# Kernel optimization log

Hardware: AMD Instinct MI355X
Metric: run time of the kernel (lower is better)

The kernel has to match this reference:

```python
import jax, jax.numpy as jnp
import numpy as np
from jax import lax

B, S, I, H, O, L = 64, 1024, 256, 1024, 256, 2


def setup_inputs() -> dict:
    key = jax.random.key(0)
    ks = iter(jax.random.split(key, 64))
    d = {}
    d["x"] = jax.random.normal(next(ks), (B, S, I), dtype=jnp.float32)
    d["h0"] = jnp.zeros((B, L, H), dtype=jnp.float32)
    for l in range(L):
        ind = I if l == 0 else H
        sx = 1.0 / np.sqrt(ind)
        sh = 1.0 / np.sqrt(H)
        d[f"Wxz_{l}"] = jax.random.uniform(next(ks), (ind, H), jnp.float32, -sx, sx)
        d[f"Wxr_{l}"] = jax.random.uniform(next(ks), (ind, H), jnp.float32, -sx, sx)
        d[f"Wxg_{l}"] = jax.random.uniform(next(ks), (ind, H), jnp.float32, -sx, sx)
        d[f"Whz_{l}"] = jax.random.uniform(next(ks), (H, H), jnp.float32, -sh, sh)
        d[f"bhz_{l}"] = jax.random.uniform(next(ks), (H,), jnp.float32, -sh, sh)
        d[f"Whr_{l}"] = jax.random.uniform(next(ks), (H, H), jnp.float32, -sh, sh)
        d[f"bhr_{l}"] = jax.random.uniform(next(ks), (H,), jnp.float32, -sh, sh)
        d[f"Whg_{l}"] = jax.random.uniform(next(ks), (H, H), jnp.float32, -sh, sh)
        d[f"bhg_{l}"] = jax.random.uniform(next(ks), (H,), jnp.float32, -sh, sh)
    sy = 1.0 / np.sqrt(H)
    d["WY"] = jax.random.uniform(next(ks), (H, O), jnp.float32, -sy, sy)
    d["bY"] = jax.random.uniform(next(ks), (O,), jnp.float32, -sy, sy)
    return d


def _gru_forward(x, h0, layer_params, WY, bY):
    # x: [B,S,I], h0: [B,L,H]
    def step(states, xt):
        inp = xt  # [B, in_dim]
        new_states = []
        for l, (wxz, wxr, wxg, whz, bhz, whr, bhr, whg, bhg) in enumerate(layer_params):
            h = states[l]
            z = jax.nn.sigmoid(inp @ wxz + h @ whz + bhz)
            r = jax.nn.sigmoid(inp @ wxr + h @ whr + bhr)
            g = jnp.tanh(inp @ wxg + (r * h) @ whg + bhg)
            h = z * h + (1.0 - z) * g
            new_states.append(h)
            inp = h  # dropout=0 -> identity
        y = inp @ WY + bY
        return tuple(new_states), y

    states0 = tuple(h0[:, l, :] for l in range(len(layer_params)))
    xs = jnp.swapaxes(x, 0, 1)  # [S,B,I]
    final_states, ys = lax.scan(step, states0, xs)
    layer_output = jnp.swapaxes(ys, 0, 1)  # [B,S,O]
    hidden_state = jnp.stack(final_states, axis=1)  # [B,L,H]
    return layer_output, hidden_state


def reference(x, h0,
              Wxz_0, Wxr_0, Wxg_0, Whz_0, bhz_0, Whr_0, bhr_0, Whg_0, bhg_0,
              Wxz_1, Wxr_1, Wxg_1, Whz_1, bhz_1, Whr_1, bhr_1, Whg_1, bhg_1,
              WY, bY):
    layer_params = [
        (Wxz_0, Wxr_0, Wxg_0, Whz_0, bhz_0, Whr_0, bhr_0, Whg_0, bhg_0),
        (Wxz_1, Wxr_1, Wxg_1, Whz_1, bhz_1, Whr_1, bhr_1, Whg_1, bhg_1),
    ]
    return _gru_forward(x, h0, layer_params, WY, bY)
```

## Files before the change

### kernel.cpp

```cpp
#include <hip/hip_runtime.h>
#include <hip/hip_bf16.h>
#include <stdint.h>


#define NWG 200
#define TPB 256

typedef unsigned long long u64;
typedef __attribute__((ext_vector_type(8))) short bfrag;
typedef __attribute__((ext_vector_type(4))) float f32x4;

constexpr int Bc = 64, Sc = 1024, Ic = 256, Hc = 1024, Oc = 256;

struct Args {
  const float *x, *h0in;
  const float *W1[7], *W2[7], *bias[7];
  unsigned short *h0[2], *h1[2], *z0[2], *rh0[2], *z1[2], *rh1[2];
  unsigned *sl;
  float *y, *hs;
};

__device__ __forceinline__ u64 ald64(const void *p) {
  return __hip_atomic_load((const u64 *)p, __ATOMIC_RELAXED, __HIP_MEMORY_SCOPE_AGENT);
}
__device__ __forceinline__ unsigned ald32(const void *p) {
  return __hip_atomic_load((const unsigned *)p, __ATOMIC_RELAXED, __HIP_MEMORY_SCOPE_AGENT);
}
__device__ __forceinline__ void ast32(void *p, unsigned v) {
  __hip_atomic_store((unsigned *)p, v, __ATOMIC_RELAXED, __HIP_MEMORY_SCOPE_AGENT);
}
__device__ __forceinline__ unsigned short f2b(float x) {
  __hip_bfloat16 b = __float2bfloat16(x);
  return __builtin_bit_cast(unsigned short, b);
}
__device__ __forceinline__ float b2f(unsigned short u) {
  return __uint_as_float(((unsigned)u) << 16);
}

__device__ void waitslots(const unsigned *sl, int pslot, int pthr) {
  __shared__ int notdone;
  while (true) {
    int bad = 0;
    if (pslot >= 0)
      bad = ((int)ald32(sl + (size_t)pslot * 32) < pthr);
    if (threadIdx.x == 0) notdone = 0;
    __syncthreads();
    if (bad) notdone = 1;
    __syncthreads();
    if (!notdone) break;
    __builtin_amdgcn_s_sleep(2);
  }
}

__device__ void stamp(unsigned *sl, int wg, unsigned v) {
  __syncthreads();
  if (threadIdx.x == 0)
    __hip_atomic_store(sl + (size_t)wg * 32, v, __ATOMIC_RELAXED, __HIP_MEMORY_SCOPE_AGENT);
}

__device__ __forceinline__ void ldb(u64 *dst, const u64 *ap, int ks) {
#pragma unroll
  for (int q = 0; q < 8; ++q) {
    dst[2 * q]     = ald64(ap + (size_t)(ks + q) * 8);
    dst[2 * q + 1] = ald64(ap + (size_t)(ks + q) * 8 + 1);
  }
}
__device__ __forceinline__ void useb(f32x4 *acc, const u64 *src, const short *wl,
                                     int nkoff, int ks, int lane) {
#pragma unroll
  for (int q = 0; q < 8; ++q) {
    union { u64 u[2]; bfrag v; } cc;
    cc.u[0] = src[2 * q]; cc.u[1] = src[2 * q + 1];
    const short *wp = wl + (((size_t)(nkoff + ks + q) * 2) * 64 + lane) * 8;
    acc[0] = __builtin_amdgcn_mfma_f32_16x16x32_bf16(cc.v, *(const bfrag *)wp, acc[0], 0, 0, 0);
    acc[1] = __builtin_amdgcn_mfma_f32_16x16x32_bf16(cc.v, *(const bfrag *)(wp + 512), acc[1], 0, 0, 0);
  }
}
__device__ void seg_h(f32x4 *acc, const unsigned short *hb, const short *wl,
                      int nkoff, int lane, int rbase) {
  const u64 *ap = (const u64 *)(hb + (size_t)(rbase + (lane & 15)) * Hc) + (lane >> 4) * 2;
  u64 A[16], B[16];
  ldb(A, ap, 0);
  ldb(B, ap, 8);
  useb(acc, A, wl, nkoff, 0, lane);
  ldb(A, ap, 16);
  useb(acc, B, wl, nkoff, 8, lane);
  ldb(B, ap, 24);
  useb(acc, A, wl, nkoff, 16, lane);
  useb(acc, B, wl, nkoff, 24, lane);
}
__device__ void seg_x(f32x4 *acc, const float *xt, const short *wl, int lane, int rbase) {
  const float4 *xp = (const float4 *)(xt + (size_t)(rbase + (lane & 15)) * Sc * Ic) + (lane >> 4) * 2;
  float4 xv[16];
#pragma unroll
  for (int q = 0; q < 8; ++q) {
    xv[2 * q]     = xp[(size_t)q * 8];
    xv[2 * q + 1] = xp[(size_t)q * 8 + 1];
  }
#pragma unroll
  for (int q = 0; q < 8; ++q) {
    bfrag av;
    const float *f0 = (const float *)&xv[2 * q];
    const float *f1 = (const float *)&xv[2 * q + 1];
#pragma unroll
    for (int e = 0; e < 4; ++e) {
      av[e]     = (short)f2b(f0[e]);
      av[4 + e] = (short)f2b(f1[e]);
    }
    const short *wp = wl + (((size_t)q * 2) * 64 + lane) * 8;
    acc[0] = __builtin_amdgcn_mfma_f32_16x16x32_bf16(av, *(const bfrag *)wp, acc[0], 0, 0, 0);
    acc[1] = __builtin_amdgcn_mfma_f32_16x16x32_bf16(av, *(const bfrag *)(wp + 512), acc[1], 0, 0, 0);
  }
}

__device__ void store_sig(unsigned short *out, f32x4 *acc, int c0, int lane, int rbase) {
#pragma unroll
  for (int nt = 0; nt < 2; ++nt) {
    int col = c0 + nt * 16 + (lane & 15);
#pragma unroll
    for (int j = 0; j < 4; ++j) {
      float v = 1.f / (1.f + expf(-acc[nt][j]));
      float vo = __shfl_xor(v, 1);
      if (!(lane & 1)) {
        int row = rbase + (lane >> 4) * 4 + j;
        ast32((unsigned *)out + (((size_t)row * Hc + col) >> 1),
              (unsigned)f2b(v) | ((unsigned)f2b(vo) << 16));
      }
    }
  }
}
__device__ void store_rh(unsigned short *out, const unsigned short *hb, f32x4 *acc,
                         int c0, int lane, int rbase) {
  unsigned hw[8];
#pragma unroll
  for (int nt = 0; nt < 2; ++nt)
#pragma unroll
    for (int j = 0; j < 4; ++j)
      if (!(lane & 1)) {
        int col = c0 + nt * 16 + (lane & 15);
        int row = rbase + (lane >> 4) * 4 + j;
        hw[nt * 4 + j] = ald32((const unsigned *)hb + (((size_t)row * Hc + col) >> 1));
      }
#pragma unroll
  for (int nt = 0; nt < 2; ++nt) {
    int col = c0 + nt * 16 + (lane & 15);
#pragma unroll
    for (int j = 0; j < 4; ++j) {
      float v = 1.f / (1.f + expf(-acc[nt][j]));
      float vo = __shfl_xor(v, 1);
      if (!(lane & 1)) {
        unsigned w = hw[nt * 4 + j];
        int row = rbase + (lane >> 4) * 4 + j;
        unsigned pk = (unsigned)f2b(v * b2f((unsigned short)(w & 0xffff)))
                    | ((unsigned)f2b(vo * b2f((unsigned short)(w >> 16))) << 16);
        ast32((unsigned *)out + (((size_t)row * Hc + col) >> 1), pk);
      }
    }
  }
}
__device__ void store_gupd(unsigned short *hnew, const unsigned short *hold,
                           const unsigned short *zb, f32x4 *acc, int c0, int lane, int rbase) {
  unsigned zw[8], hw[8];
#pragma unroll
  for (int nt = 0; nt < 2; ++nt)
#pragma unroll
    for (int j = 0; j < 4; ++j)
      if (!(lane & 1)) {
        int col = c0 + nt * 16 + (lane & 15);
        size_t iw = ((size_t)(rbase + (lane >> 4) * 4 + j) * Hc + col) >> 1;
        zw[nt * 4 + j] = ald32((const unsigned *)zb + iw);
        hw[nt * 4 + j] = ald32((const unsigned *)hold + iw);
      }
#pragma unroll
  for (int nt = 0; nt < 2; ++nt) {
    int col = c0 + nt * 16 + (lane & 15);
#pragma unroll
    for (int j = 0; j < 4; ++j) {
      float g = tanhf(acc[nt][j]);
      float go = __shfl_xor(g, 1);
      if (!(lane & 1)) {
        unsigned wz = zw[nt * 4 + j], wh = hw[nt * 4 + j];
        float zl = b2f((unsigned short)(wz & 0xffff)), zh = b2f((unsigned short)(wz >> 16));
        float hl = b2f((unsigned short)(wh & 0xffff)), hh = b2f((unsigned short)(wh >> 16));
        float hn0 = zl * hl + (1.f - zl) * g;
        float hn1 = zh * hh + (1.f - zh) * go;
        size_t iw = ((size_t)(rbase + (lane >> 4) * 4 + j) * Hc + col) >> 1;
        ast32((unsigned *)hnew + iw, (unsigned)f2b(hn0) | ((unsigned)f2b(hn1) << 16));
      }
    }
  }
}

__device__ void pack_weights(short *wl, const float *W1, int K1, int ld1,
                             const float *W2, int K2, int ld2, int c0) {
  int NK = (K1 + K2) / 32;
  for (int slot = threadIdx.x; slot < NK * 128; slot += TPB) {
    int ks = slot >> 7, rem = slot & 127, nt = rem >> 6, ln = rem & 63;
    int c = c0 + nt * 16 + (ln & 15);
    int k0 = ks * 32 + (ln >> 4) * 8;
    short *dst = wl + (((size_t)ks * 2 + nt) * 64 + ln) * 8;
#pragma unroll
    for (int j = 0; j < 8; ++j) {
      int k = k0 + j;
      float w = (k < K1) ? W1[(size_t)k * ld1 + c] : W2[(size_t)(k - K1) * ld2 + c];
      dst[j] = (short)f2b(w);
    }
  }
}

__global__ void __launch_bounds__(TPB) gru_df(Args a) {
  extern __shared__ short wl[];
  const int wg = blockIdx.x, tid = threadIdx.x;
  const int lane = tid & 63, wid = tid >> 6, rbase = wid * 16;
  const int gate = (wg < 32) ? 0 : (wg < 64) ? 1 : (wg < 96) ? 2 :
                   (wg < 128) ? 3 : (wg < 160) ? 4 : (wg < 192) ? 5 : 6;
  const int c0 = (gate == 6) ? (wg - 192) * 32 : (wg - gate * 32) * 32;
  static const int K1tab[7] = {256, 256, 256, 1024, 1024, 1024, 1024};
  static const int K2tab[7] = {1024, 1024, 1024, 1024, 1024, 1024, 0};
  const int ld1 = (gate == 6) ? Oc : Hc;

  pack_weights(wl, a.W1[gate], K1tab[gate], ld1, a.W2[gate], K2tab[gate], Hc, c0);

  int pslot = -1, poff = 0;
  if (gate <= 1) {
    if (tid < 32) { pslot = 64 + tid; poff = 1; }
  } else if (gate == 2) {
    if (tid < 64)       { pslot = tid;              poff = 2; }
    else if (tid < 128) { pslot = 96 + (tid - 64);  poff = 0; }
    else if (tid < 160) { pslot = 160 + (tid - 128); poff = 0; }
  } else if (gate <= 4) {
    if (tid < 32)      { pslot = 64 + tid;          poff = 2; }
    else if (tid < 64) { pslot = 160 + (tid - 32);  poff = 1; }
  } else if (gate == 5) {
    if (tid < 64)       { pslot = 96 + tid;         poff = 2; }
    else if (tid < 96)  { pslot = 64 + (tid - 64);  poff = 2; }
    else if (tid < 104) { pslot = 192 + (tid - 96); poff = 0; }
  } else {
    if (tid < 32) { pslot = 160 + tid; poff = 2; }
  }

  for (int u = wg * TPB + tid; u < Bc * Hc / 2; u += NWG * TPB) {
    int b = u >> 9, hp = (u & 511) * 2;
    const float *s0 = a.h0in + (size_t)(b * 2) * Hc + hp;
    const float *s1 = a.h0in + (size_t)(b * 2 + 1) * Hc + hp;
    ast32((unsigned *)a.h0[1] + u, (unsigned)f2b(s0[0]) | ((unsigned)f2b(s0[1]) << 16));
    ast32((unsigned *)a.h1[1] + u, (unsigned)f2b(s1[0]) | ((unsigned)f2b(s1[1]) << 16));
  }
  stamp(a.sl, wg, 1);
  waitslots(a.sl, (tid < NWG) ? tid : -1, 1);

  const float *bias = a.bias[gate];

  if (gate <= 1) {
    for (int t = 0; t < Sc; ++t) {
      waitslots(a.sl, pslot, (pslot >= 0) ? t + poff : 0);
      const unsigned short *h0c = a.h0[(t + 1) & 1];
      float b0 = bias[c0 + (lane & 15)], b1 = bias[c0 + 16 + (lane & 15)];
      f32x4 acc[2] = {{b0, b0, b0, b0}, {b1, b1, b1, b1}};
      seg_x(acc, a.x + (size_t)t * Ic, wl, lane, rbase);
      seg_h(acc, h0c, wl, 8, lane, rbase);
      if (gate == 0) store_sig(a.z0[t & 1], acc, c0, lane, rbase);
      else           store_rh(a.rh0[t & 1], h0c, acc, c0, lane, rbase);
      stamp(a.sl, wg, t + 2);
    }
  } else if (gate == 2) {
    for (int t = 0; t < Sc; ++t) {
      waitslots(a.sl, pslot, (pslot >= 0) ? t + poff : 0);
      const unsigned short *h0c = a.h0[(t + 1) & 1];
      unsigned short *h0n = a.h0[t & 1];
      float b0 = bias[c0 + (lane & 15)], b1 = bias[c0 + 16 + (lane & 15)];
      f32x4 acc[2] = {{b0, b0, b0, b0}, {b1, b1, b1, b1}};
      seg_x(acc, a.x + (size_t)t * Ic, wl, lane, rbase);
      seg_h(acc, a.rh0[t & 1], wl, 8, lane, rbase);
      store_gupd(h0n, h0c, a.z0[t & 1], acc, c0, lane, rbase);
      stamp(a.sl, wg, t + 2);
    }
    {
      int eslot = -1;
      if (tid < 32) eslot = 64 + tid;
      else if (tid < 64) eslot = 160 + (tid - 32);
      waitslots(a.sl, eslot, Sc + 1);
    }
    for (int k = (wg - 64) * TPB + tid; k < Bc * 2 * Hc; k += 32 * TPB) {
      int b = k >> 11, l = (k >> 10) & 1, h = k & 1023;
      const unsigned short *src = l ? a.h1[1] : a.h0[1];
      size_t idx = (size_t)b * Hc + h;
      unsigned wv = ald32((const unsigned *)src + idx / 2);
      a.hs[k] = b2f((unsigned short)((h & 1) ? (wv >> 16) : (wv & 0xffff)));
    }
  } else if (gate <= 4) {
    for (int t = 0; t < Sc; ++t) {
      waitslots(a.sl, pslot, (pslot >= 0) ? t + poff : 0);
      const unsigned short *h0n = a.h0[t & 1];
      const unsigned short *h1c = a.h1[(t + 1) & 1];
      float b0 = bias[c0 + (lane & 15)], b1 = bias[c0 + 16 + (lane & 15)];
      f32x4 acc[2] = {{b0, b0, b0, b0}, {b1, b1, b1, b1}};
      seg_h(acc, h0n, wl, 0, lane, rbase);
      seg_h(acc, h1c, wl, 32, lane, rbase);
      if (gate == 3) store_sig(a.z1[t & 1], acc, c0, lane, rbase);
      else           store_rh(a.rh1[t & 1], h1c, acc, c0, lane, rbase);
      stamp(a.sl, wg, t + 2);
    }
  } else if (gate == 5) {
    for (int t = 0; t < Sc; ++t) {
      waitslots(a.sl, pslot, (pslot >= 0) ? t + poff : 0);
      const unsigned short *h0n = a.h0[t & 1];
      const unsigned short *h1c = a.h1[(t + 1) & 1];
      unsigned short *h1n = a.h1[t & 1];
      float b0 = bias[c0 + (lane & 15)], b1 = bias[c0 + 16 + (lane & 15)];
      f32x4 acc[2] = {{b0, b0, b0, b0}, {b1, b1, b1, b1}};
      seg_h(acc, h0n, wl, 0, lane, rbase);
      seg_h(acc, a.rh1[t & 1], wl, 32, lane, rbase);
      store_gupd(h1n, h1c, a.z1[t & 1], acc, c0, lane, rbase);
      stamp(a.sl, wg, t + 2);
    }
  } else {
    for (int t = 0; t < Sc; ++t) {
      waitslots(a.sl, pslot, (pslot >= 0) ? t + poff : 0);
      const unsigned short *h1t = a.h1[t & 1];
      float b0 = bias[c0 + (lane & 15)], b1 = bias[c0 + 16 + (lane & 15)];
      f32x4 acc[2] = {{b0, b0, b0, b0}, {b1, b1, b1, b1}};
      seg_h(acc, h1t, wl, 0, lane, rbase);
#pragma unroll
      for (int nt = 0; nt < 2; ++nt) {
        int col = c0 + nt * 16 + (lane & 15);
#pragma unroll
        for (int j = 0; j < 4; ++j) {
          int row = rbase + (lane >> 4) * 4 + j;
          a.y[((size_t)row * Sc + t) * Oc + col] = acc[nt][j];
        }
      }
      stamp(a.sl, wg, t + 2);
    }
  }
}

extern "C" void kernel_launch(void *const *d_in, const int *in_sizes, int n_in,
                              void *d_out, int out_size, void *d_ws, size_t ws_size,
                              hipStream_t stream) {
  (void)in_sizes; (void)n_in; (void)out_size; (void)ws_size;
  Args a;
  a.x    = (const float *)d_in[0];
  a.h0in = (const float *)d_in[1];
  a.W1[0] = (const float *)d_in[2];  a.W2[0] = (const float *)d_in[5];  a.bias[0] = (const float *)d_in[6];
  a.W1[1] = (const float *)d_in[3];  a.W2[1] = (const float *)d_in[7];  a.bias[1] = (const float *)d_in[8];
  a.W1[2] = (const float *)d_in[4];  a.W2[2] = (const float *)d_in[9];  a.bias[2] = (const float *)d_in[10];
  a.W1[3] = (const float *)d_in[11]; a.W2[3] = (const float *)d_in[14]; a.bias[3] = (const float *)d_in[15];
  a.W1[4] = (const float *)d_in[12]; a.W2[4] = (const float *)d_in[16]; a.bias[4] = (const float *)d_in[17];
  a.W1[5] = (const float *)d_in[13]; a.W2[5] = (const float *)d_in[18]; a.bias[5] = (const float *)d_in[19];
  a.W1[6] = (const float *)d_in[20]; a.W2[6] = nullptr;                 a.bias[6] = (const float *)d_in[21];

  char *w = (char *)d_ws;
  a.h0[0]  = (unsigned short *)(w + 0);
  a.h0[1]  = (unsigned short *)(w + 131072);
  a.h1[0]  = (unsigned short *)(w + 262144);
  a.h1[1]  = (unsigned short *)(w + 393216);
  a.z0[0]  = (unsigned short *)(w + 524288);
  a.z0[1]  = (unsigned short *)(w + 655360);
  a.rh0[0] = (unsigned short *)(w + 786432);
  a.rh0[1] = (unsigned short *)(w + 917504);
  a.z1[0]  = (unsigned short *)(w + 1048576);
  a.z1[1]  = (unsigned short *)(w + 1179648);
  a.rh1[0] = (unsigned short *)(w + 1310720);
  a.rh1[1] = (unsigned short *)(w + 1441792);
  a.sl     = (unsigned *)(w + 1572864);
  a.y   = (float *)d_out;
  a.hs  = a.y + (size_t)Bc * Sc * Oc;

  (void)hipMemsetAsync(a.sl, 0, 32768, stream);
  (void)hipFuncSetAttribute((const void *)gru_df,
                            hipFuncAttributeMaxDynamicSharedMemorySize, 131072);
  gru_df<<<NWG, TPB, 131072, stream>>>(a);
}
```

Measured before the change: 41.92 ms.

## Store recurrent bf16 state buffers in k-octet-major tiled layout

```diff
diff --git a/kernel.cpp b/kernel.cpp
--- a/kernel.cpp
+++ b/kernel.cpp
@@ -35,6 +35,9 @@
 }
 __device__ __forceinline__ float b2f(unsigned short u) {
   return __uint_as_float(((unsigned)u) << 16);
+}
+__device__ __forceinline__ size_t tidx32(int row, int col) {
+  return ((size_t)(col >> 3) * 64 + row) * 4 + ((col & 7) >> 1);
 }
 
 __device__ void waitslots(const unsigned *sl, int pslot, int pthr) {
@@ -51,7 +54,6 @@
     __builtin_amdgcn_s_sleep(2);
   }
 }
-
 __device__ void stamp(unsigned *sl, int wg, unsigned v) {
   __syncthreads();
   if (threadIdx.x == 0)
@@ -61,8 +63,8 @@
 __device__ __forceinline__ void ldb(u64 *dst, const u64 *ap, int ks) {
 #pragma unroll
   for (int q = 0; q < 8; ++q) {
-    dst[2 * q]     = ald64(ap + (size_t)(ks + q) * 8);
-    dst[2 * q + 1] = ald64(ap + (size_t)(ks + q) * 8 + 1);
+    dst[2 * q]     = ald64(ap + (size_t)(ks + q) * 512);
+    dst[2 * q + 1] = ald64(ap + (size_t)(ks + q) * 512 + 1);
   }
 }
 __device__ __forceinline__ void useb(f32x4 *acc, const u64 *src, const short *wl,
@@ -78,7 +80,8 @@
 }
 __device__ void seg_h(f32x4 *acc, const unsigned short *hb, const short *wl,
                       int nkoff, int lane, int rbase) {
-  const u64 *ap = (const u64 *)(hb + (size_t)(rbase + (lane & 15)) * Hc) + (lane >> 4) * 2;
+  const u64 *ap = (const u64 *)hb +
+                  ((size_t)((lane >> 4) * 64 + rbase + (lane & 15)) * 2);
   u64 A[16], B[16];
   ldb(A, ap, 0);
   ldb(B, ap, 8);
@@ -123,7 +126,7 @@
       float vo = __shfl_xor(v, 1);
       if (!(lane & 1)) {
         int row = rbase + (lane >> 4) * 4 + j;
-        ast32((unsigned *)out + (((size_t)row * Hc + col) >> 1),
+        ast32((unsigned *)out + tidx32(row, col),
               (unsigned)f2b(v) | ((unsigned)f2b(vo) << 16));
       }
     }
@@ -139,7 +142,7 @@
       if (!(lane & 1)) {
         int col = c0 + nt * 16 + (lane & 15);
         int row = rbase + (lane >> 4) * 4 + j;
-        hw[nt * 4 + j] = ald32((const unsigned *)hb + (((size_t)row * Hc + col) >> 1));
+        hw[nt * 4 + j] = ald32((const unsigned *)hb + tidx32(row, col));
       }
 #pragma unroll
   for (int nt = 0; nt < 2; ++nt) {
@@ -153,7 +156,7 @@
         int row = rbase + (lane >> 4) * 4 + j;
         unsigned pk = (unsigned)f2b(v * b2f((unsigned short)(w & 0xffff)))
                     | ((unsigned)f2b(vo * b2f((unsigned short)(w >> 16))) << 16);
-        ast32((unsigned *)out + (((size_t)row * Hc + col) >> 1), pk);
+        ast32((unsigned *)out + tidx32(row, col), pk);
       }
     }
   }
@@ -167,7 +170,7 @@
     for (int j = 0; j < 4; ++j)
       if (!(lane & 1)) {
         int col = c0 + nt * 16 + (lane & 15);
-        size_t iw = ((size_t)(rbase + (lane >> 4) * 4 + j) * Hc + col) >> 1;
+        size_t iw = tidx32(rbase + (lane >> 4) * 4 + j, col);
         zw[nt * 4 + j] = ald32((const unsigned *)zb + iw);
         hw[nt * 4 + j] = ald32((const unsigned *)hold + iw);
       }
@@ -184,8 +187,8 @@
         float hl = b2f((unsigned short)(wh & 0xffff)), hh = b2f((unsigned short)(wh >> 16));
         float hn0 = zl * hl + (1.f - zl) * g;
         float hn1 = zh * hh + (1.f - zh) * go;
-        size_t iw = ((size_t)(rbase + (lane >> 4) * 4 + j) * Hc + col) >> 1;
-        ast32((unsigned *)hnew + iw, (unsigned)f2b(hn0) | ((unsigned)f2b(hn1) << 16));
+        ast32((unsigned *)hnew + tidx32(rbase + (lane >> 4) * 4 + j, col),
+              (unsigned)f2b(hn0) | ((unsigned)f2b(hn1) << 16));
       }
     }
   }
@@ -240,9 +243,11 @@
   }
 
   for (int u = wg * TPB + tid; u < Bc * Hc / 2; u += NWG * TPB) {
-    int b = u >> 9, hp = (u & 511) * 2;
-    const float *s0 = a.h0in + (size_t)(b * 2) * Hc + hp;
-    const float *s1 = a.h0in + (size_t)(b * 2 + 1) * Hc + hp;
+    int tile = u >> 2, word = u & 3;
+    int b = tile & 63, oct = tile >> 6;
+    int c = oct * 8 + word * 2;
+    const float *s0 = a.h0in + (size_t)(b * 2) * Hc + c;
+    const float *s1 = a.h0in + (size_t)(b * 2 + 1) * Hc + c;
     ast32((unsigned *)a.h0[1] + u, (unsigned)f2b(s0[0]) | ((unsigned)f2b(s0[1]) << 16));
     ast32((unsigned *)a.h1[1] + u, (unsigned)f2b(s1[0]) | ((unsigned)f2b(s1[1]) << 16));
   }
@@ -284,8 +289,8 @@
     for (int k = (wg - 64) * TPB + tid; k < Bc * 2 * Hc; k += 32 * TPB) {
       int b = k >> 11, l = (k >> 10) & 1, h = k & 1023;
       const unsigned short *src = l ? a.h1[1] : a.h0[1];
-      size_t idx = (size_t)b * Hc + h;
-      unsigned wv = ald32((const unsigned *)src + idx / 2);
+      size_t i16 = ((size_t)(h >> 3) * 64 + b) * 8 + (h & 7);
+      unsigned wv = ald32((const unsigned *)src + (i16 >> 1));
       a.hs[k] = b2f((unsigned short)((h & 1) ? (wv >> 16) : (wv & 0xffff)));
     }
   } else if (gate <= 4) {
```

After: 37.77 ms. 1.11x faster.
